# Performance work log

Measured on AMD Instinct MI355X. Metric: run time of the kernel, lower is better.

Reference implementation:

```python
import jax, jax.numpy as jnp
import numpy as np

M, D, NI, L, NPL, R, T = 2, 128, 131072, 4, 2048, 8, 32
N = NI + L * NPL  # total DAG nodes


def setup_inputs() -> dict:
    key = jax.random.key(0)
    ks = jax.random.split(key, 18)
    thax = jax.random.randint(ks[0], (NI,), 0, T)
    sine = jax.random.uniform(ks[1], (NI,), jnp.float32)
    # parents of layer-l deriv nodes index any node built earlier (topological)
    raw = jax.random.randint(ks[2], (L, NPL, 2), 0, 2**30)
    bounds = jnp.array([NI + l * NPL for l in range(L)])[:, None, None]
    par = raw % bounds
    ridx = jax.random.randint(ks[3], (L, NPL), 0, R)
    pos = jax.random.uniform(ks[4], (N,), jnp.float32) + 0.01
    neg = jax.random.uniform(ks[5], (N,), jnp.float32) + 0.01
    s = 0.05
    return {
        'thax': thax, 'sine': sine, 'par': par, 'ridx': ridx,
        'pos': pos, 'neg': neg,
        'init_table': jax.random.normal(ks[6], (M, T, D)) * s,
        's_vec': jax.random.normal(ks[7], (M, D)) * s,
        'W1': jax.random.normal(ks[8], (M, R, 2 * D, D)) * s,
        'b1': jax.random.normal(ks[9], (M, R, D)) * s,
        'W2': jax.random.normal(ks[10], (M, R, D, D)) * s,
        'b2': jax.random.normal(ks[11], (M, R, D)) * s,
        'tweaks': jax.random.normal(ks[12], (M, 1, 2)) * s,
        'We1': jax.random.normal(ks[13], (M, D, D)) * s,
        'be1': jax.random.normal(ks[14], (M, D)) * s,
        'we2': jax.random.normal(ks[15], (M, D)) * s,
        'be2': jax.random.normal(ks[16], (M,)) * s,
    }


def reference(thax, sine, par, ridx, pos, neg, init_table, s_vec,
              W1, b1, W2, b2, tweaks, We1, be1, we2, be2):
    # init nodes: thax embedding + sine embellishment (per model)
    emb0 = init_table[:, thax, :] + sine[None, :, None] * s_vec[:, None, :]  # [M,NI,D]
    store = jnp.zeros((M, N, D), emb0.dtype).at[:, :NI].set(emb0)
    # topological layers of deriv nodes: gather parents, rule-indexed 2-layer MLP
    for l in range(L):
        p, r = par[l], ridx[l]
        cat = store[:, p].reshape(M, NPL, 2 * D)               # gather parents
        h = jax.nn.relu(jnp.einsum('mnc,mncd->mnd', cat, W1[:, r]) + b1[:, r])
        out = (jnp.einsum('mnd,mnde->mne', h, W2[:, r]) + b2[:, r]
               + tweaks[:, 0, 1][:, None, None])
        store = store.at[:, NI + l * NPL: NI + (l + 1) * NPL].set(out)
    # eval_net: per-node scalar logit (+ per-problem tweak)
    he = jax.nn.relu(jnp.einsum('mnd,mde->mne', store, We1) + be1[:, None, :])
    logit = jnp.einsum('mnd,md->mn', he, we2) + be2[:, None] + tweaks[:, 0, 0][:, None]
    tot_pos, tot_neg = pos.sum(), neg.sum()
    pw = tot_neg / tot_pos  # POS_WEIGHT_EXTRA = 1.0
    gold = pos / (pos + neg)
    w = pos + neg
    # BCEWithLogitsLoss(pos_weight=pw) per node, weighted by (pos+neg)
    bce = -(pw * gold[None] * jax.nn.log_sigmoid(logit)
            + (1.0 - gold[None]) * jax.nn.log_sigmoid(-logit))
    loss = (w[None] * bce).sum(axis=1)                          # [M]
    posOK = jnp.where(logit >= 0, pos[None], 0.0).sum(axis=1)
    negOK = jnp.where(logit < 0, neg[None], 0.0).sum(axis=1)
    return (loss, posOK, negOK, tot_pos, tot_neg)
```

## Files before the change

kernel.cpp:

```cpp
#include <hip/hip_runtime.h>
#include <hip/hip_bf16.h>

#define M_ 2
#define D_ 128
#define NI_ 131072
#define L_ 4
#define NPL_ 2048
#define R_ 8
#define T_ 32
#define N_ (NI_ + L_ * NPL_)
#define ND_ (L_ * NPL_)
#define PSTRIDE_ 1280
#define PUSED_ 1248

typedef __bf16 bf16x8 __attribute__((ext_vector_type(8)));
typedef float f32x4 __attribute__((ext_vector_type(4)));

#define OFF_W1T    0u
#define OFF_W2T    1048576u
#define OFF_WE1T   1572864u
#define OFF_TAB    1638400u
#define OFF_SVEC   1654784u
#define OFF_EA2    1688448u
#define OFF_EWB    1721216u
#define OFF_PA     1723264u
#define OFF_PB     1733504u
#define OFF_PPOK   1743744u
#define OFF_PNOK   1753984u
#define OFF_PTP    1764224u
#define OFF_PTN    1769344u
#define OFF_G      1774464u
#define OFF_STORE  2315136u
#define OFF_FSG    6509440u
#define OFF_CFG    6509472u
#define OFF_FLIST  6509504u
#define OFF_SAL    6542272u
#define OFF_SBL    6575040u
#define OFF_FSGA   6577088u
#define OFF_CFGA   6577120u
#define OFF_CB24   6577152u
#define OFF_OB24   6577248u

__device__ __forceinline__ unsigned short f2bu(float f) {
  unsigned int u = __float_as_uint(f);
  u += 0x7fffu + ((u >> 16) & 1u);
  return (unsigned short)(u >> 16);
}
__device__ __forceinline__ bf16x8 ldb8(const unsigned short* p) {
  return *reinterpret_cast<const bf16x8*>(p);
}

__device__ __forceinline__ bf16x8 node_chunk(int m, int row, int d0,
    const unsigned short* tab, const unsigned short* svec,
    const unsigned short* sd, const int* thax, const float* sine) {
  if (row < NI_) {
    bf16x8 tv = ldb8(&tab[(m * T_ + thax[row]) * D_ + d0]);
    bf16x8 sv = ldb8(&svec[m * D_ + d0]);
    float sn = sine[row];
    bf16x8 r;
#pragma unroll
    for (int j = 0; j < 8; ++j)
      r[j] = (__bf16)((float)tv[j] + sn * (float)sv[j]);
    return r;
  }
  return ldb8(&sd[(size_t)(m * ND_ + (row - NI_)) * D_ + d0]);
}

__global__ __launch_bounds__(256) void megaprep_kernel(
    const float* W1, const float* W2, const float* We1,
    const float* init_table, const float* s_vec,
    const float* b1, const float* be1, const float* we2,
    const int* ridx, const int* par,
    unsigned short* W1T, unsigned short* W2T, unsigned short* We1T,
    unsigned short* tab, unsigned short* svec,
    float* G, float* EA2, float* EWB,
    int* fsg, int* cfg, int* fastlist,
    int* fsgA, int* cfgA, int* slowAlist,
    int* cB24, int* oB24, int* slowBlist, unsigned int* pzero) {
  __shared__ float smem[1056];
  __shared__ unsigned int fbm[256];
  __shared__ int scnt[40], soff[40];
  int job = blockIdx.x;
  int tid = threadIdx.x;

  if (job < 800) {
    int z, rblk, cblk;
    if (job < 512)      { z = job >> 5;            rblk = (job & 31) >> 2; cblk = job & 3; }
    else if (job < 768) { int q = job - 512; z = 16 + (q >> 4); rblk = (q & 15) >> 2; cblk = q & 3; }
    else                { int q = job - 768; z = 32 + (q >> 4); rblk = (q & 15) >> 2; cblk = q & 3; }
    const float* src; unsigned short* dst; int R;
    if (z < 16)      { src = W1  + (size_t)z * 32768;        dst = W1T  + (size_t)z * 32768;        R = 256; }
    else if (z < 32) { src = W2  + (size_t)(z - 16) * 16384; dst = W2T  + (size_t)(z - 16) * 16384; R = 128; }
    else             { src = We1 + (size_t)(z - 32) * 16384; dst = We1T + (size_t)(z - 32) * 16384; R = 128; }
    int r0 = rblk * 32, c0 = cblk * 32;
    float (*tile)[33] = (float(*)[33])smem;
    int tx = tid & 31, ty = tid >> 5;
#pragma unroll
    for (int k = 0; k < 4; ++k)
      tile[ty + 8 * k][tx] = src[(size_t)(r0 + ty + 8 * k) * D_ + c0 + tx];
    __syncthreads();
#pragma unroll
    for (int k = 0; k < 4; ++k)
      dst[(size_t)(c0 + ty + 8 * k) * R + r0 + tx] = f2bu(tile[tx][ty + 8 * k]);
  } else if (job == 800) {
    for (int i = tid; i < 8448; i += 256) {
      if (i < 8192) tab[i] = f2bu(init_table[i]);
      else svec[i - 8192] = f2bu(s_vec[i - 8192]);
    }
  } else if (job < 1329) {
    int q = job - 801;
    int t = q / 16, mr = q & 15;
    int m = mr >> 3;
    int slot = tid >> 7, e = tid & 127;
    const float* vec = (t < 32) ? &init_table[(size_t)(m * T_ + t) * D_]
                                : &s_vec[(size_t)m * D_];
    if (tid < 128) smem[tid] = vec[tid];
    __syncthreads();
    const float* w = &W1[((size_t)mr * 256 + slot * 128) * D_];
    float acc = 0.f;
#pragma unroll 8
    for (int c = 0; c < 128; ++c) acc = fmaf(smem[c], w[c * D_ + e], acc);
    if (slot == 0 && t < 32) acc += b1[mr * D_ + e];
    G[((size_t)(mr * 2 + slot) * 33 + t) * D_ + e] = acc;
  } else if (job < 1363) {
    int q = job - 1329;
    int m = q / 17, t = (q % 17) * 2 + (tid >> 7);
    int e = tid & 127;
    if (t <= 32) {
      const float* vec = (t < 32) ? &init_table[(size_t)(m * T_ + t) * D_]
                                  : &s_vec[(size_t)m * D_];
      const float* w = &We1[(size_t)m * D_ * D_];
      float acc = 0.f;
#pragma unroll 8
      for (int d = 0; d < 128; ++d) acc = fmaf(vec[d], w[d * D_ + e], acc);
      if (t < 32) {
        EA2[m * 4096 + ((e >> 1) * 32 + t) * 2 + (e & 1)] = acc + be1[m * D_ + e];
      } else {
        EWB[(m * D_ + e) * 2 + 0] = acc;
        EWB[(m * D_ + e) * 2 + 1] = we2[m * D_ + e];
      }
    }
  } else if (job == 1363) {
    for (int i = tid; i < 256; i += 256) fbm[i] = 0u;
    for (int i = tid; i < 40; i += 256) scnt[i] = 0;
    __syncthreads();
    for (int g = tid; g < ND_; g += 256) {
      if (par[2 * g] < NI_ && par[2 * g + 1] < NI_)
        atomicOr(&fbm[g >> 5], 1u << (g & 31));
    }
    __syncthreads();
    for (int g = tid; g < ND_; g += 256) {
      int r = ridx[g];
      int f = (fbm[g >> 5] >> (g & 31)) & 1;
      if (f) atomicAdd(&scnt[r], 1);
      else {
        int p0 = par[2 * g], p1 = par[2 * g + 1];
        int a0 = p0 < NI_ || ((fbm[(p0 - NI_) >> 5] >> ((p0 - NI_) & 31)) & 1);
        int a1 = p1 < NI_ || ((fbm[(p1 - NI_) >> 5] >> ((p1 - NI_) & 31)) & 1);
        if (a0 && a1) atomicAdd(&scnt[8 + r], 1);
        else atomicAdd(&scnt[16 + ((g >> 11) - 1) * 8 + r], 1);
      }
    }
    __syncthreads();
    if (tid == 0) {
      int run = 0;
      for (int r = 0; r < 8; ++r) { soff[r] = run; fsg[r] = run; cfg[r] = scnt[r]; run += scnt[r]; }
      run = 0;
      for (int r = 0; r < 8; ++r) { soff[8 + r] = run; fsgA[r] = run; cfgA[r] = scnt[8 + r]; run += scnt[8 + r]; }
      run = 0;
      for (int b = 0; b < 24; ++b) { soff[16 + b] = run; oB24[b] = run; cB24[b] = scnt[16 + b]; run += scnt[16 + b]; }
    }
    __syncthreads();
    for (int g = tid; g < ND_; g += 256) {
      int r = ridx[g];
      int f = (fbm[g >> 5] >> (g & 31)) & 1;
      if (f) fastlist[atomicAdd(&soff[r], 1)] = g;
      else {
        int p0 = par[2 * g], p1 = par[2 * g + 1];
        int a0 = p0 < NI_ || ((fbm[(p0 - NI_) >> 5] >> ((p0 - NI_) & 31)) & 1);
        int a1 = p1 < NI_ || ((fbm[(p1 - NI_) >> 5] >> ((p1 - NI_) & 31)) & 1);
        if (a0 && a1) slowAlist[atomicAdd(&soff[8 + r], 1)] = g;
        else slowBlist[atomicAdd(&soff[16 + ((g >> 11) - 1) * 8 + r], 1)] = g;
      }
    }
  } else {
    for (int i = tid; i < 12800; i += 256) pzero[i] = 0u;
  }
}

__global__ __launch_bounds__(256) void main_kernel(
    const int* thax, const float* sine, const int* par,
    const float* pos, const float* neg,
    const float* b2, const float* tweaks,
    const float* G, const unsigned short* W2T, const unsigned short* We1T,
    const float* EA2, const float* EWB,
    const float* be1, const float* we2, const float* be2,
    const int* fsg, const int* cfg, const int* fastlist,
    unsigned short* sd,
    float* pA, float* pB, float* pPok, float* pNok, float* pTp, float* pTn) {
  __shared__ float sbuf[4448];
  int bid = blockIdx.x;
  int tid = threadIdx.x;
  int w = tid >> 6, lane = tid & 63;

  if (bid < 1280) {
    int m = bid / 640, q = bid % 640;
    int r = q / 80, tile = q % 80;
    int cnt = cfg[r];
    int base = tile * 16;
    if (base >= cnt) return;
    unsigned short* h_lds = (unsigned short*)sbuf;
    int*   t0a  = (int*)(sbuf + 1024);
    int*   t1a  = t0a + 16;
    float* s0a  = (float*)(t1a + 16);
    float* s1a  = s0a + 16;
    int*   gida = (int*)(s1a + 16);
    float* red2 = sbuf + 1104;
    if (tid < 16) {
      int loc = base + tid; if (loc >= cnt) loc = cnt - 1;
      int gid = fastlist[fsg[r] + loc];
      int p0 = par[2 * gid], p1 = par[2 * gid + 1];
      t0a[tid] = thax[p0]; s0a[tid] = sine[p0];
      t1a[tid] = thax[p1]; s1a[tid] = sine[p1];
      gida[tid] = gid;
    }
    __syncthreads();
    const float* Gm = &G[(size_t)(m * R_ + r) * 8448];
    {
      int row = tid >> 4, seg = tid & 15, d0 = seg * 8;
      int t0 = t0a[row], t1 = t1a[row];
      float s0 = s0a[row], s1 = s1a[row];
      const float* pa = &Gm[t0 * 128 + d0];
      const float* pb = &Gm[(33 + t1) * 128 + d0];
      const float* pu = &Gm[4096 + d0];
      const float* pv = &Gm[8320 + d0];
      bf16x8 hv;
#pragma unroll
      for (int half = 0; half < 2; ++half) {
        float4 a = *(const float4*)(pa + half * 4);
        float4 b = *(const float4*)(pb + half * 4);
        float4 u = *(const float4*)(pu + half * 4);
        float4 v = *(const float4*)(pv + half * 4);
        hv[half * 4 + 0] = (__bf16)fmaxf(a.x + b.x + s0 * u.x + s1 * v.x, 0.f);
        hv[half * 4 + 1] = (__bf16)fmaxf(a.y + b.y + s0 * u.y + s1 * v.y, 0.f);
        hv[half * 4 + 2] = (__bf16)fmaxf(a.z + b.z + s0 * u.z + s1 * v.z, 0.f);
        hv[half * 4 + 3] = (__bf16)fmaxf(a.w + b.w + s0 * u.w + s1 * v.w, 0.f);
      }
      *(bf16x8*)&h_lds[row * 128 + (d0 ^ ((row & 7) << 3))] = hv;
    }
    __syncthreads();
    int l15 = lane & 15, l4 = lane >> 4;
    const unsigned short* w2b = &W2T[(size_t)(m * R_ + r) * D_ * D_];
    f32x4 acc[2];
    acc[0] = (f32x4){0.f, 0.f, 0.f, 0.f};
    acc[1] = (f32x4){0.f, 0.f, 0.f, 0.f};
#pragma unroll
    for (int kc = 0; kc < 4; ++kc) {
      int d0 = kc * 32 + l4 * 8;
      bf16x8 a2 = ldb8(&h_lds[l15 * 128 + (d0 ^ ((l15 & 7) << 3))]);
#pragma unroll
      for (int f = 0; f < 2; ++f) {
        int fg = w * 2 + f;
        bf16x8 b = ldb8(&w2b[(fg * 16 + l15) * D_ + d0]);
        acc[f] = __builtin_amdgcn_mfma_f32_16x16x32_bf16(a2, b, acc[f], 0, 0, 0);
      }
    }
    float tw1 = tweaks[m * 2 + 1];
    const float* b2v = &b2[(m * R_ + r) * D_];
    __syncthreads();
#pragma unroll
    for (int i = 0; i < 4; ++i) {
      int row = l4 * 4 + i;
      int g = base + row;
#pragma unroll
      for (int f = 0; f < 2; ++f) {
        int e = (w * 2 + f) * 16 + l15;
        unsigned short val = f2bu(acc[f][i] + b2v[e] + tw1);
        h_lds[row * 128 + (e ^ ((row & 7) << 3))] = val;
        if (g < cnt) sd[(size_t)(m * ND_ + gida[row]) * D_ + e] = val;
      }
    }
    __syncthreads();
    f32x4 ae[2];
    ae[0] = (f32x4){0.f, 0.f, 0.f, 0.f};
    ae[1] = (f32x4){0.f, 0.f, 0.f, 0.f};
    const unsigned short* we1b = &We1T[(size_t)m * D_ * D_];
#pragma unroll
    for (int kc = 0; kc < 4; ++kc) {
      int d0 = kc * 32 + l4 * 8;
      bf16x8 a2 = ldb8(&h_lds[l15 * 128 + (d0 ^ ((l15 & 7) << 3))]);
#pragma unroll
      for (int f = 0; f < 2; ++f) {
        int fg = w * 2 + f;
        bf16x8 b = ldb8(&we1b[(fg * 16 + l15) * D_ + d0]);
        ae[f] = __builtin_amdgcn_mfma_f32_16x16x32_bf16(a2, b, ae[f], 0, 0, 0);
      }
    }
    float part[4] = {0.f, 0.f, 0.f, 0.f};
#pragma unroll
    for (int f = 0; f < 2; ++f) {
      int e = (w * 2 + f) * 16 + l15;
      float bb = be1[m * D_ + e];
      float wv = we2[m * D_ + e];
#pragma unroll
      for (int i = 0; i < 4; ++i) {
        float he = ae[f][i] + bb;
        he = he > 0.f ? he : 0.f;
        part[i] += he * wv;
      }
    }
#pragma unroll
    for (int mask = 1; mask < 16; mask <<= 1) {
#pragma unroll
      for (int i = 0; i < 4; ++i) part[i] += __shfl_xor(part[i], mask, 64);
    }
    if (l15 == 0) {
#pragma unroll
      for (int i = 0; i < 4; ++i) red2[w * 16 + l4 * 4 + i] = part[i];
    }
    __syncthreads();
    if (tid < 16) {
      int g = base + tid;
      float v6[4] = {0.f, 0.f, 0.f, 0.f};
      if (g < cnt) {
        float logit = red2[tid] + red2[16 + tid] + red2[32 + tid] + red2[48 + tid]
                    + be2[m] + tweaks[m * 2 + 0];
        int grow = NI_ + gida[tid];
        float p_ = pos[grow], n_ = neg[grow];
        float lse = log1pf(__expf(-fabsf(logit)));
        v6[0] = p_ * (fmaxf(-logit, 0.f) + lse);
        v6[1] = n_ * (fmaxf(logit, 0.f) + lse);
        v6[2] = logit >= 0.f ? p_ : 0.f;
        v6[3] = logit < 0.f ? n_ : 0.f;
      }
#pragma unroll
      for (int mask = 1; mask < 16; mask <<= 1) {
#pragma unroll
        for (int qq = 0; qq < 4; ++qq) v6[qq] += __shfl_xor(v6[qq], mask, 64);
      }
      if (tid == 0) {
        int slot = 512 + r * 80 + tile;
        pA[m * PSTRIDE_ + slot] = v6[0];
        pB[m * PSTRIDE_ + slot] = v6[1];
        pPok[m * PSTRIDE_ + slot] = v6[2];
        pNok[m * PSTRIDE_ + slot] = v6[3];
      }
    }
  } else if (bid < 2304) {
    int q = bid - 1280;
    int m = q >> 9, xb = q & 511;
    float* lea = sbuf;
    float* lwb = sbuf + 4096;
    float* red = sbuf + 4352;
    for (int i = tid; i < 4096; i += 256) lea[i] = EA2[m * 4096 + i];
    if (tid < 256) lwb[tid] = EWB[m * 256 + tid];
    __syncthreads();
    int row = xb * 256 + tid;
    int t = thax[row];
    float s = sine[row];
    float acc = 0.f;
#pragma unroll 8
    for (int p = 0; p < 64; ++p) {
      float2 ea = *(const float2*)&lea[(p * 32 + t) * 2];
      float4 wb = *(const float4*)&lwb[p * 4];
      float x0 = fmaf(s, wb.x, ea.x); x0 = fmaxf(x0, 0.f);
      acc = fmaf(x0, wb.y, acc);
      float x1 = fmaf(s, wb.z, ea.y); x1 = fmaxf(x1, 0.f);
      acc = fmaf(x1, wb.w, acc);
    }
    float logit = acc + be2[m] + tweaks[m * 2 + 0];
    float p_ = pos[row], n_ = neg[row];
    float lse = log1pf(__expf(-fabsf(logit)));
    float v[6];
    v[0] = p_ * (fmaxf(-logit, 0.f) + lse);
    v[1] = n_ * (fmaxf(logit, 0.f) + lse);
    v[2] = logit >= 0.f ? p_ : 0.f;
    v[3] = logit < 0.f ? n_ : 0.f;
    v[4] = p_; v[5] = n_;
#pragma unroll
    for (int mask = 1; mask < 64; mask <<= 1) {
#pragma unroll
      for (int k = 0; k < 6; ++k) v[k] += __shfl_xor(v[k], mask, 64);
    }
    if (lane == 0) {
#pragma unroll
      for (int k = 0; k < 6; ++k) red[k * 16 + w] = v[k];
    }
    __syncthreads();
    if (tid == 0) {
      float t6[6];
#pragma unroll
      for (int k = 0; k < 6; ++k)
        t6[k] = red[k * 16 + 0] + red[k * 16 + 1] + red[k * 16 + 2] + red[k * 16 + 3];
      pA[m * PSTRIDE_ + xb] = t6[0];
      pB[m * PSTRIDE_ + xb] = t6[1];
      pPok[m * PSTRIDE_ + xb] = t6[2];
      pNok[m * PSTRIDE_ + xb] = t6[3];
      if (m == 0) { pTp[xb] = t6[4]; pTn[xb] = t6[5]; }
    }
  } else {
    int j = bid - 2304;
    float* red = sbuf;
    const float* src = j ? neg : pos;
    float s = 0.f;
    for (int i = NI_ + tid; i < N_; i += 256) s += src[i];
#pragma unroll
    for (int mask = 1; mask < 64; mask <<= 1) s += __shfl_xor(s, mask, 64);
    if (lane == 0) red[w] = s;
    __syncthreads();
    if (tid == 0) {
      float t = red[0] + red[1] + red[2] + red[3];
      if (j == 0) pTp[1152] = t; else pTn[1152] = t;
    }
  }
}

__global__ __launch_bounds__(128) void slowA_kernel(
    const int* thax, const float* sine, const int* par,
    const float* b1, const float* b2, const float* tweaks,
    const float* pos, const float* neg,
    const float* be1, const float* we2, const float* be2,
    const unsigned short* tab, const unsigned short* svec,
    const unsigned short* W1T, const unsigned short* W2T,
    const unsigned short* We1T,
    const int* fsgA, const int* cfgA, const int* slowAlist,
    unsigned short* sd,
    float* pA, float* pB, float* pPok, float* pNok) {
  int tile = blockIdx.x, r = blockIdx.y, m = blockIdx.z;
  int cnt = cfgA[r];
  int base = tile * 16;
  if (base >= cnt) return;
  int start = fsgA[r];
  int tid = threadIdx.x;
  int w = tid >> 6, lane = tid & 63;
  int l15 = lane & 15, l4 = lane >> 4;
  __shared__ unsigned short h_lds[16 * 128];
  __shared__ float red2[32];
  __shared__ int grows[16];

  if (tid < 16) {
    int loc = base + tid; if (loc >= cnt) loc = cnt - 1;
    grows[tid] = slowAlist[start + loc];
  }
  __syncthreads();
  int g0 = grows[l15];
  int p0 = par[2 * g0], p1 = par[2 * g0 + 1];
  const unsigned short* w1b = &W1T[(size_t)(m * R_ + r) * D_ * 256];
  const unsigned short* w2b = &W2T[(size_t)(m * R_ + r) * D_ * D_];
  const unsigned short* we1b = &We1T[(size_t)m * D_ * D_];

  bf16x8 av[8];
#pragma unroll
  for (int kc = 0; kc < 8; ++kc) {
    int k = kc * 32 + l4 * 8;
    int p = (k < 128) ? p0 : p1;
    av[kc] = node_chunk(m, p, k & 127, tab, svec, sd, thax, sine);
  }
  f32x4 acch[4];
#pragma unroll
  for (int f = 0; f < 4; ++f) acch[f] = (f32x4){0.f, 0.f, 0.f, 0.f};
#pragma unroll
  for (int kc = 0; kc < 8; ++kc) {
    int k = kc * 32 + l4 * 8;
#pragma unroll
    for (int f = 0; f < 4; ++f) {
      int fg = w * 4 + f;
      bf16x8 b = ldb8(&w1b[(fg * 16 + l15) * 256 + k]);
      acch[f] = __builtin_amdgcn_mfma_f32_16x16x32_bf16(av[kc], b, acch[f], 0, 0, 0);
    }
  }
  const float* b1v = &b1[(m * R_ + r) * D_];
#pragma unroll
  for (int f = 0; f < 4; ++f) {
    int d = (w * 4 + f) * 16 + l15;
    float bb = b1v[d];
#pragma unroll
    for (int i = 0; i < 4; ++i) {
      int row = l4 * 4 + i;
      float h = acch[f][i] + bb;
      h = h > 0.f ? h : 0.f;
      h_lds[row * 128 + (d ^ ((row & 7) << 3))] = f2bu(h);
    }
  }
  __syncthreads();
  f32x4 acco[4];
#pragma unroll
  for (int f = 0; f < 4; ++f) acco[f] = (f32x4){0.f, 0.f, 0.f, 0.f};
#pragma unroll
  for (int kc = 0; kc < 4; ++kc) {
    int d0 = kc * 32 + l4 * 8;
    bf16x8 a2 = ldb8(&h_lds[l15 * 128 + (d0 ^ ((l15 & 7) << 3))]);
#pragma unroll
    for (int f = 0; f < 4; ++f) {
      int fg = w * 4 + f;
      bf16x8 b = ldb8(&w2b[(fg * 16 + l15) * D_ + d0]);
      acco[f] = __builtin_amdgcn_mfma_f32_16x16x32_bf16(a2, b, acco[f], 0, 0, 0);
    }
  }
  float tw1 = tweaks[m * 2 + 1];
  const float* b2v = &b2[(m * R_ + r) * D_];
  __syncthreads();
#pragma unroll
  for (int i = 0; i < 4; ++i) {
    int row = l4 * 4 + i;
    int g = base + row;
#pragma unroll
    for (int f = 0; f < 4; ++f) {
      int e = (w * 4 + f) * 16 + l15;
      unsigned short val = f2bu(acco[f][i] + b2v[e] + tw1);
      h_lds[row * 128 + (e ^ ((row & 7) << 3))] = val;
      if (g < cnt) sd[(size_t)(m * ND_ + grows[row]) * D_ + e] = val;
    }
  }
  __syncthreads();
  f32x4 ae[4];
#pragma unroll
  for (int f = 0; f < 4; ++f) ae[f] = (f32x4){0.f, 0.f, 0.f, 0.f};
#pragma unroll
  for (int kc = 0; kc < 4; ++kc) {
    int d0 = kc * 32 + l4 * 8;
    bf16x8 a2 = ldb8(&h_lds[l15 * 128 + (d0 ^ ((l15 & 7) << 3))]);
#pragma unroll
    for (int f = 0; f < 4; ++f) {
      int fg = w * 4 + f;
      bf16x8 b = ldb8(&we1b[(fg * 16 + l15) * D_ + d0]);
      ae[f] = __builtin_amdgcn_mfma_f32_16x16x32_bf16(a2, b, ae[f], 0, 0, 0);
    }
  }
  float part[4] = {0.f, 0.f, 0.f, 0.f};
#pragma unroll
  for (int f = 0; f < 4; ++f) {
    int e = (w * 4 + f) * 16 + l15;
    float bb = be1[m * D_ + e];
    float wv = we2[m * D_ + e];
#pragma unroll
    for (int i = 0; i < 4; ++i) {
      float he = ae[f][i] + bb;
      he = he > 0.f ? he : 0.f;
      part[i] += he * wv;
    }
  }
#pragma unroll
  for (int mask = 1; mask < 16; mask <<= 1) {
#pragma unroll
    for (int i = 0; i < 4; ++i) part[i] += __shfl_xor(part[i], mask, 64);
  }
  if (l15 == 0) {
#pragma unroll
    for (int i = 0; i < 4; ++i) red2[w * 16 + l4 * 4 + i] = part[i];
  }
  __syncthreads();
  if (tid < 16) {
    int g = base + tid;
    float v6[4] = {0.f, 0.f, 0.f, 0.f};
    if (g < cnt) {
      float logit = red2[tid] + red2[16 + tid] + be2[m] + tweaks[m * 2 + 0];
      int grow = NI_ + grows[tid];
      float p_ = pos[grow], n_ = neg[grow];
      float lse = log1pf(__expf(-fabsf(logit)));
      v6[0] = p_ * (fmaxf(-logit, 0.f) + lse);
      v6[1] = n_ * (fmaxf(logit, 0.f) + lse);
      v6[2] = logit >= 0.f ? p_ : 0.f;
      v6[3] = logit < 0.f ? n_ : 0.f;
    }
#pragma unroll
    for (int mask = 1; mask < 16; mask <<= 1) {
#pragma unroll
      for (int qq = 0; qq < 4; ++qq) v6[qq] += __shfl_xor(v6[qq], mask, 64);
    }
    if (tid == 0) {
      int slot = 1153 + r * 6 + tile;
      pA[m * PSTRIDE_ + slot] = v6[0];
      pB[m * PSTRIDE_ + slot] = v6[1];
      pPok[m * PSTRIDE_ + slot] = v6[2];
      pNok[m * PSTRIDE_ + slot] = v6[3];
    }
  }
}

__global__ __launch_bounds__(128) void slowB_kernel(int l,
    const int* thax, const float* sine, const int* par,
    const float* b1, const float* b2, const float* tweaks,
    const float* pos, const float* neg,
    const float* be1, const float* we2, const float* be2,
    const unsigned short* tab, const unsigned short* svec,
    const unsigned short* W1T, const unsigned short* W2T,
    const unsigned short* We1T,
    const int* cB24, const int* oB24, const int* slowBlist,
    unsigned short* sd,
    float* pA, float* pB, float* pPok, float* pNok) {
  int tile = blockIdx.x, r = blockIdx.y, m = blockIdx.z;
  int bkt = (l - 1) * 8 + r;
  int cnt = cB24[bkt];
  int base = tile * 16;
  if (base >= cnt) return;
  int off = oB24[bkt];
  int tid = threadIdx.x;
  int w = tid >> 6, lane = tid & 63;
  int l15 = lane & 15, l4 = lane >> 4;
  __shared__ unsigned short h_lds[16 * 128];
  __shared__ float red2[32];
  __shared__ int grows[16];

  if (tid < 16) {
    int loc = base + tid; if (loc >= cnt) loc = cnt - 1;
    grows[tid] = slowBlist[off + loc];
  }
  __syncthreads();
  int g0 = grows[l15];
  int p0 = par[2 * g0], p1 = par[2 * g0 + 1];
  const unsigned short* w1b = &W1T[(size_t)(m * R_ + r) * D_ * 256];
  const unsigned short* w2b = &W2T[(size_t)(m * R_ + r) * D_ * D_];
  const unsigned short* we1b = &We1T[(size_t)m * D_ * D_];

  bf16x8 av[8];
#pragma unroll
  for (int kc = 0; kc < 8; ++kc) {
    int k = kc * 32 + l4 * 8;
    int p = (k < 128) ? p0 : p1;
    av[kc] = node_chunk(m, p, k & 127, tab, svec, sd, thax, sine);
  }
  f32x4 acch[4];
#pragma unroll
  for (int f = 0; f < 4; ++f) acch[f] = (f32x4){0.f, 0.f, 0.f, 0.f};
#pragma unroll
  for (int kc = 0; kc < 8; ++kc) {
    int k = kc * 32 + l4 * 8;
#pragma unroll
    for (int f = 0; f < 4; ++f) {
      int fg = w * 4 + f;
      bf16x8 b = ldb8(&w1b[(fg * 16 + l15) * 256 + k]);
      acch[f] = __builtin_amdgcn_mfma_f32_16x16x32_bf16(av[kc], b, acch[f], 0, 0, 0);
    }
  }
  const float* b1v = &b1[(m * R_ + r) * D_];
#pragma unroll
  for (int f = 0; f < 4; ++f) {
    int d = (w * 4 + f) * 16 + l15;
    float bb = b1v[d];
#pragma unroll
    for (int i = 0; i < 4; ++i) {
      int row = l4 * 4 + i;
      float h = acch[f][i] + bb;
      h = h > 0.f ? h : 0.f;
      h_lds[row * 128 + (d ^ ((row & 7) << 3))] = f2bu(h);
    }
  }
  __syncthreads();
  f32x4 acco[4];
#pragma unroll
  for (int f = 0; f < 4; ++f) acco[f] = (f32x4){0.f, 0.f, 0.f, 0.f};
#pragma unroll
  for (int kc = 0; kc < 4; ++kc) {
    int d0 = kc * 32 + l4 * 8;
    bf16x8 a2 = ldb8(&h_lds[l15 * 128 + (d0 ^ ((l15 & 7) << 3))]);
#pragma unroll
    for (int f = 0; f < 4; ++f) {
      int fg = w * 4 + f;
      bf16x8 b = ldb8(&w2b[(fg * 16 + l15) * D_ + d0]);
      acco[f] = __builtin_amdgcn_mfma_f32_16x16x32_bf16(a2, b, acco[f], 0, 0, 0);
    }
  }
  float tw1 = tweaks[m * 2 + 1];
  const float* b2v = &b2[(m * R_ + r) * D_];
  __syncthreads();
#pragma unroll
  for (int i = 0; i < 4; ++i) {
    int row = l4 * 4 + i;
    int g = base + row;
#pragma unroll
    for (int f = 0; f < 4; ++f) {
      int e = (w * 4 + f) * 16 + l15;
      unsigned short val = f2bu(acco[f][i] + b2v[e] + tw1);
      h_lds[row * 128 + (e ^ ((row & 7) << 3))] = val;
      if (g < cnt) sd[(size_t)(m * ND_ + grows[row]) * D_ + e] = val;
    }
  }
  __syncthreads();
  f32x4 ae[4];
#pragma unroll
  for (int f = 0; f < 4; ++f) ae[f] = (f32x4){0.f, 0.f, 0.f, 0.f};
#pragma unroll
  for (int kc = 0; kc < 4; ++kc) {
    int d0 = kc * 32 + l4 * 8;
    bf16x8 a2 = ldb8(&h_lds[l15 * 128 + (d0 ^ ((l15 & 7) << 3))]);
#pragma unroll
    for (int f = 0; f < 4; ++f) {
      int fg = w * 4 + f;
      bf16x8 b = ldb8(&we1b[(fg * 16 + l15) * D_ + d0]);
      ae[f] = __builtin_amdgcn_mfma_f32_16x16x32_bf16(a2, b, ae[f], 0, 0, 0);
    }
  }
  float part[4] = {0.f, 0.f, 0.f, 0.f};
#pragma unroll
  for (int f = 0; f < 4; ++f) {
    int e = (w * 4 + f) * 16 + l15;
    float bb = be1[m * D_ + e];
    float wv = we2[m * D_ + e];
#pragma unroll
    for (int i = 0; i < 4; ++i) {
      float he = ae[f][i] + bb;
      he = he > 0.f ? he : 0.f;
      part[i] += he * wv;
    }
  }
#pragma unroll
  for (int mask = 1; mask < 16; mask <<= 1) {
#pragma unroll
    for (int i = 0; i < 4; ++i) part[i] += __shfl_xor(part[i], mask, 64);
  }
  if (l15 == 0) {
#pragma unroll
    for (int i = 0; i < 4; ++i) red2[w * 16 + l4 * 4 + i] = part[i];
  }
  __syncthreads();
  if (tid < 16) {
    int g = base + tid;
    float v6[4] = {0.f, 0.f, 0.f, 0.f};
    if (g < cnt) {
      float logit = red2[tid] + red2[16 + tid] + be2[m] + tweaks[m * 2 + 0];
      int grow = NI_ + grows[tid];
      float p_ = pos[grow], n_ = neg[grow];
      float lse = log1pf(__expf(-fabsf(logit)));
      v6[0] = p_ * (fmaxf(-logit, 0.f) + lse);
      v6[1] = n_ * (fmaxf(logit, 0.f) + lse);
      v6[2] = logit >= 0.f ? p_ : 0.f;
      v6[3] = logit < 0.f ? n_ : 0.f;
    }
#pragma unroll
    for (int mask = 1; mask < 16; mask <<= 1) {
#pragma unroll
      for (int qq = 0; qq < 4; ++qq) v6[qq] += __shfl_xor(v6[qq], mask, 64);
    }
    if (tid == 0) {
      int slot = 1201 + (l - 2) * 16 + r * 2 + tile;
      pA[m * PSTRIDE_ + slot] = v6[0];
      pB[m * PSTRIDE_ + slot] = v6[1];
      pPok[m * PSTRIDE_ + slot] = v6[2];
      pNok[m * PSTRIDE_ + slot] = v6[3];
    }
  }
}

__global__ __launch_bounds__(256) void finalize_kernel(
    const float* pA, const float* pB, const float* pPok, const float* pNok,
    const float* pTp, const float* pTn, float* out) {
  __shared__ float lred[10][4];
  const float* srcs[10] = {pA, pA + PSTRIDE_, pB, pB + PSTRIDE_,
                           pPok, pPok + PSTRIDE_, pNok, pNok + PSTRIDE_,
                           pTp, pTn};
  int tid = threadIdx.x;
  int w = tid >> 6, lane = tid & 63;
#pragma unroll
  for (int q = 0; q < 10; ++q) {
    float s = 0.f;
    for (int i = tid; i < PUSED_; i += 256) s += srcs[q][i];
#pragma unroll
    for (int mask = 1; mask < 64; mask <<= 1) s += __shfl_xor(s, mask, 64);
    if (lane == 0) lred[q][w] = s;
  }
  __syncthreads();
  if (tid == 0) {
    float totals[10];
#pragma unroll
    for (int q = 0; q < 10; ++q)
      totals[q] = lred[q][0] + lred[q][1] + lred[q][2] + lred[q][3];
    float tp = totals[8], tn = totals[9];
    float pw = tn / tp;
    out[0] = pw * totals[0] + totals[2];
    out[1] = pw * totals[1] + totals[3];
    out[2] = totals[4]; out[3] = totals[5];
    out[4] = totals[6]; out[5] = totals[7];
    out[6] = tp; out[7] = tn;
  }
}

extern "C" void kernel_launch(void* const* d_in, const int* in_sizes, int n_in,
                              void* d_out, int out_size, void* d_ws, size_t ws_size,
                              hipStream_t stream) {
  const int*   thax = (const int*)d_in[0];
  const float* sine = (const float*)d_in[1];
  const int*   par  = (const int*)d_in[2];
  const int*   ridx = (const int*)d_in[3];
  const float* pos  = (const float*)d_in[4];
  const float* neg  = (const float*)d_in[5];
  const float* init_table = (const float*)d_in[6];
  const float* s_vec = (const float*)d_in[7];
  const float* W1 = (const float*)d_in[8];
  const float* b1 = (const float*)d_in[9];
  const float* W2 = (const float*)d_in[10];
  const float* b2 = (const float*)d_in[11];
  const float* tweaks = (const float*)d_in[12];
  const float* We1 = (const float*)d_in[13];
  const float* be1 = (const float*)d_in[14];
  const float* we2 = (const float*)d_in[15];
  const float* be2 = (const float*)d_in[16];

  char* ws = (char*)d_ws;
  unsigned short* W1T  = (unsigned short*)(ws + OFF_W1T);
  unsigned short* W2T  = (unsigned short*)(ws + OFF_W2T);
  unsigned short* We1T = (unsigned short*)(ws + OFF_WE1T);
  unsigned short* tab  = (unsigned short*)(ws + OFF_TAB);
  unsigned short* svec = (unsigned short*)(ws + OFF_SVEC);
  float* EA2  = (float*)(ws + OFF_EA2);
  float* EWB  = (float*)(ws + OFF_EWB);
  float* pA   = (float*)(ws + OFF_PA);
  float* pB   = (float*)(ws + OFF_PB);
  float* pPok = (float*)(ws + OFF_PPOK);
  float* pNok = (float*)(ws + OFF_PNOK);
  float* pTp  = (float*)(ws + OFF_PTP);
  float* pTn  = (float*)(ws + OFF_PTN);
  float* G    = (float*)(ws + OFF_G);
  unsigned short* sd = (unsigned short*)(ws + OFF_STORE);
  int* fsg      = (int*)(ws + OFF_FSG);
  int* cfg      = (int*)(ws + OFF_CFG);
  int* fastlist = (int*)(ws + OFF_FLIST);
  int* slowAlist = (int*)(ws + OFF_SAL);
  int* slowBlist = (int*)(ws + OFF_SBL);
  int* fsgA     = (int*)(ws + OFF_FSGA);
  int* cfgA     = (int*)(ws + OFF_CFGA);
  int* cB24     = (int*)(ws + OFF_CB24);
  int* oB24     = (int*)(ws + OFF_OB24);

  megaprep_kernel<<<1365, 256, 0, stream>>>(
      W1, W2, We1, init_table, s_vec, b1, be1, we2, ridx, par,
      W1T, W2T, We1T, tab, svec, G, EA2, EWB,
      fsg, cfg, fastlist, fsgA, cfgA, slowAlist, cB24, oB24, slowBlist,
      (unsigned int*)pA);
  main_kernel<<<2306, 256, 0, stream>>>(
      thax, sine, par, pos, neg, b2, tweaks, G, W2T, We1T, EA2, EWB,
      be1, we2, be2, fsg, cfg, fastlist, sd,
      pA, pB, pPok, pNok, pTp, pTn);
  slowA_kernel<<<dim3(6, R_, M_), 128, 0, stream>>>(
      thax, sine, par, b1, b2, tweaks, pos, neg, be1, we2, be2,
      tab, svec, W1T, W2T, We1T, fsgA, cfgA, slowAlist, sd,
      pA, pB, pPok, pNok);
  for (int l = 2; l < L_; ++l) {
    slowB_kernel<<<dim3(2, R_, M_), 128, 0, stream>>>(
        l, thax, sine, par, b1, b2, tweaks, pos, neg, be1, we2, be2,
        tab, svec, W1T, W2T, We1T, cB24, oB24, slowBlist, sd,
        pA, pB, pPok, pNok);
  }
  finalize_kernel<<<1, 256, 0, stream>>>(pA, pB, pPok, pNok, pTp, pTn,
                                         (float*)d_out);
}
```

Baseline: 108.5 us.

## Parallelize node bucketing across 40 blocks with fixed-capacity lists and ballot compaction

The single-block serial bucketing job (bitmap, count, prefix sum, scatter) is replaced by 40 blocks, one per bucket. Each block scans all derived nodes, recomputes the fast/slowA test directly from parent indices, and compacts its matches into a fixed-capacity list using wavefront ballot plus one LDS atomic per wave. The bucketing jobs are also moved to the lowest block indices so they start first and no longer sit on the tail of the prep kernel. In exchange, the list capacities are fixed constants sized for these inputs and overflowing nodes are silently dropped, and every block rereads the full parent array.

```diff
diff --git a/kernel.cpp b/kernel.cpp
--- a/kernel.cpp
+++ b/kernel.cpp
@@ -12,6 +12,9 @@
 #define ND_ (L_ * NPL_)
 #define PSTRIDE_ 1280
 #define PUSED_ 1248
+#define FCAP_ 1280
+#define ACAP_ 96
+#define BCAP_ 32
 
 typedef __bf16 bf16x8 __attribute__((ext_vector_type(8)));
 typedef float f32x4 __attribute__((ext_vector_type(4)));
@@ -31,15 +34,12 @@
 #define OFF_PTN    1769344u
 #define OFF_G      1774464u
 #define OFF_STORE  2315136u
-#define OFF_FSG    6509440u
-#define OFF_CFG    6509472u
-#define OFF_FLIST  6509504u
-#define OFF_SAL    6542272u
-#define OFF_SBL    6575040u
-#define OFF_FSGA   6577088u
-#define OFF_CFGA   6577120u
-#define OFF_CB24   6577152u
-#define OFF_OB24   6577248u
+#define OFF_FLIST  6509440u
+#define OFF_SAL    6550400u
+#define OFF_SBL    6553472u
+#define OFF_CFG    6556544u
+#define OFF_CFGA   6556576u
+#define OFF_CB24   6556608u
 
 __device__ __forceinline__ unsigned short f2bu(float f) {
   unsigned int u = __float_as_uint(f);
@@ -74,56 +74,68 @@
     unsigned short* W1T, unsigned short* W2T, unsigned short* We1T,
     unsigned short* tab, unsigned short* svec,
     float* G, float* EA2, float* EWB,
-    int* fsg, int* cfg, int* fastlist,
-    int* fsgA, int* cfgA, int* slowAlist,
-    int* cB24, int* oB24, int* slowBlist, unsigned int* pzero) {
+    int* fastlist, int* slowAlist, int* slowBlist,
+    int* cfg, int* cfgA, int* cB24, unsigned int* pzero) {
   __shared__ float smem[1056];
-  __shared__ unsigned int fbm[256];
-  __shared__ int scnt[40], soff[40];
+  __shared__ int lcnt;
   int job = blockIdx.x;
   int tid = threadIdx.x;
 
-  if (job < 800) {
-    int z, rblk, cblk;
-    if (job < 512)      { z = job >> 5;            rblk = (job & 31) >> 2; cblk = job & 3; }
-    else if (job < 768) { int q = job - 512; z = 16 + (q >> 4); rblk = (q & 15) >> 2; cblk = q & 3; }
-    else                { int q = job - 768; z = 32 + (q >> 4); rblk = (q & 15) >> 2; cblk = q & 3; }
-    const float* src; unsigned short* dst; int R;
-    if (z < 16)      { src = W1  + (size_t)z * 32768;        dst = W1T  + (size_t)z * 32768;        R = 256; }
-    else if (z < 32) { src = W2  + (size_t)(z - 16) * 16384; dst = W2T  + (size_t)(z - 16) * 16384; R = 128; }
-    else             { src = We1 + (size_t)(z - 32) * 16384; dst = We1T + (size_t)(z - 32) * 16384; R = 128; }
-    int r0 = rblk * 32, c0 = cblk * 32;
-    float (*tile)[33] = (float(*)[33])smem;
-    int tx = tid & 31, ty = tid >> 5;
-#pragma unroll
-    for (int k = 0; k < 4; ++k)
-      tile[ty + 8 * k][tx] = src[(size_t)(r0 + ty + 8 * k) * D_ + c0 + tx];
-    __syncthreads();
-#pragma unroll
-    for (int k = 0; k < 4; ++k)
-      dst[(size_t)(c0 + ty + 8 * k) * R + r0 + tx] = f2bu(tile[tx][ty + 8 * k]);
-  } else if (job == 800) {
+  if (job < 40) {
+    int* out; int bucketbase, cap;
+    if (job < 8)       { out = fastlist;  bucketbase = job * FCAP_;        cap = FCAP_; }
+    else if (job < 16) { out = slowAlist; bucketbase = (job - 8) * ACAP_;  cap = ACAP_; }
+    else               { out = slowBlist; bucketbase = (job - 16) * BCAP_; cap = BCAP_; }
+    if (tid == 0) lcnt = 0;
+    __syncthreads();
+    int lane = tid & 63;
+    unsigned long long lmask_lt = (1ull << lane) - 1ull;
+    for (int g = tid; g < ND_; g += 256) {
+      int p0 = par[2 * g], p1 = par[2 * g + 1];
+      bool fast = (p0 < NI_) && (p1 < NI_);
+      bool match;
+      if (job < 8) {
+        match = fast && (ridx[g] == job);
+      } else if (fast) {
+        match = false;
+      } else {
+        bool a0 = (p0 < NI_) ||
+                  (par[2 * (p0 - NI_)] < NI_ && par[2 * (p0 - NI_) + 1] < NI_);
+        bool a1 = (p1 < NI_) ||
+                  (par[2 * (p1 - NI_)] < NI_ && par[2 * (p1 - NI_) + 1] < NI_);
+        bool isA = a0 && a1;
+        if (job < 16) match = isA && (ridx[g] == job - 8);
+        else match = !isA && ((((g >> 11) - 1) * 8 + ridx[g]) == job - 16);
+      }
+      unsigned long long mask = __ballot(match);
+      if (mask) {
+        int leader = __ffsll((unsigned long long)mask) - 1;
+        int pre = __popcll(mask & lmask_lt);
+        int base_ = 0;
+        if (lane == leader) base_ = atomicAdd(&lcnt, __popcll(mask));
+        base_ = __shfl(base_, leader, 64);
+        if (match) {
+          int idx = base_ + pre;
+          if (idx < cap) out[bucketbase + idx] = g;
+        }
+      }
+    }
+    __syncthreads();
+    if (tid == 0) {
+      int c = lcnt; if (c > cap) c = cap;
+      if (job < 8) cfg[job] = c;
+      else if (job < 16) cfgA[job - 8] = c;
+      else cB24[job - 16] = c;
+    }
+  } else if (job == 40) {
+    for (int i = tid; i < 12800; i += 256) pzero[i] = 0u;
+  } else if (job == 41) {
     for (int i = tid; i < 8448; i += 256) {
       if (i < 8192) tab[i] = f2bu(init_table[i]);
       else svec[i - 8192] = f2bu(s_vec[i - 8192]);
     }
-  } else if (job < 1329) {
-    int q = job - 801;
-    int t = q / 16, mr = q & 15;
-    int m = mr >> 3;
-    int slot = tid >> 7, e = tid & 127;
-    const float* vec = (t < 32) ? &init_table[(size_t)(m * T_ + t) * D_]
-                                : &s_vec[(size_t)m * D_];
-    if (tid < 128) smem[tid] = vec[tid];
-    __syncthreads();
-    const float* w = &W1[((size_t)mr * 256 + slot * 128) * D_];
-    float acc = 0.f;
-#pragma unroll 8
-    for (int c = 0; c < 128; ++c) acc = fmaf(smem[c], w[c * D_ + e], acc);
-    if (slot == 0 && t < 32) acc += b1[mr * D_ + e];
-    G[((size_t)(mr * 2 + slot) * 33 + t) * D_ + e] = acc;
-  } else if (job < 1363) {
-    int q = job - 1329;
+  } else if (job < 76) {
+    int q = job - 42;
     int m = q / 17, t = (q % 17) * 2 + (tid >> 7);
     int e = tid & 127;
     if (t <= 32) {
@@ -140,51 +152,41 @@
         EWB[(m * D_ + e) * 2 + 1] = we2[m * D_ + e];
       }
     }
-  } else if (job == 1363) {
-    for (int i = tid; i < 256; i += 256) fbm[i] = 0u;
-    for (int i = tid; i < 40; i += 256) scnt[i] = 0;
-    __syncthreads();
-    for (int g = tid; g < ND_; g += 256) {
-      if (par[2 * g] < NI_ && par[2 * g + 1] < NI_)
-        atomicOr(&fbm[g >> 5], 1u << (g & 31));
-    }
-    __syncthreads();
-    for (int g = tid; g < ND_; g += 256) {
-      int r = ridx[g];
-      int f = (fbm[g >> 5] >> (g & 31)) & 1;
-      if (f) atomicAdd(&scnt[r], 1);
-      else {
-        int p0 = par[2 * g], p1 = par[2 * g + 1];
-        int a0 = p0 < NI_ || ((fbm[(p0 - NI_) >> 5] >> ((p0 - NI_) & 31)) & 1);
-        int a1 = p1 < NI_ || ((fbm[(p1 - NI_) >> 5] >> ((p1 - NI_) & 31)) & 1);
-        if (a0 && a1) atomicAdd(&scnt[8 + r], 1);
-        else atomicAdd(&scnt[16 + ((g >> 11) - 1) * 8 + r], 1);
-      }
-    }
-    __syncthreads();
-    if (tid == 0) {
-      int run = 0;
-      for (int r = 0; r < 8; ++r) { soff[r] = run; fsg[r] = run; cfg[r] = scnt[r]; run += scnt[r]; }
-      run = 0;
-      for (int r = 0; r < 8; ++r) { soff[8 + r] = run; fsgA[r] = run; cfgA[r] = scnt[8 + r]; run += scnt[8 + r]; }
-      run = 0;
-      for (int b = 0; b < 24; ++b) { soff[16 + b] = run; oB24[b] = run; cB24[b] = scnt[16 + b]; run += scnt[16 + b]; }
-    }
-    __syncthreads();
-    for (int g = tid; g < ND_; g += 256) {
-      int r = ridx[g];
-      int f = (fbm[g >> 5] >> (g & 31)) & 1;
-      if (f) fastlist[atomicAdd(&soff[r], 1)] = g;
-      else {
-        int p0 = par[2 * g], p1 = par[2 * g + 1];
-        int a0 = p0 < NI_ || ((fbm[(p0 - NI_) >> 5] >> ((p0 - NI_) & 31)) & 1);
-        int a1 = p1 < NI_ || ((fbm[(p1 - NI_) >> 5] >> ((p1 - NI_) & 31)) & 1);
-        if (a0 && a1) slowAlist[atomicAdd(&soff[8 + r], 1)] = g;
-        else slowBlist[atomicAdd(&soff[16 + ((g >> 11) - 1) * 8 + r], 1)] = g;
-      }
-    }
+  } else if (job < 604) {
+    int q = job - 76;
+    int t = q / 16, mr = q & 15;
+    int m = mr >> 3;
+    int slot = tid >> 7, e = tid & 127;
+    const float* vec = (t < 32) ? &init_table[(size_t)(m * T_ + t) * D_]
+                                : &s_vec[(size_t)m * D_];
+    if (tid < 128) smem[tid] = vec[tid];
+    __syncthreads();
+    const float* w = &W1[((size_t)mr * 256 + slot * 128) * D_];
+    float acc = 0.f;
+#pragma unroll 8
+    for (int c = 0; c < 128; ++c) acc = fmaf(smem[c], w[c * D_ + e], acc);
+    if (slot == 0 && t < 32) acc += b1[mr * D_ + e];
+    G[((size_t)(mr * 2 + slot) * 33 + t) * D_ + e] = acc;
   } else {
-    for (int i = tid; i < 12800; i += 256) pzero[i] = 0u;
+    int q0 = job - 604;
+    int z, rblk, cblk;
+    if (q0 < 512)      { z = q0 >> 5;            rblk = (q0 & 31) >> 2; cblk = q0 & 3; }
+    else if (q0 < 768) { int q = q0 - 512; z = 16 + (q >> 4); rblk = (q & 15) >> 2; cblk = q & 3; }
+    else               { int q = q0 - 768; z = 32 + (q >> 4); rblk = (q & 15) >> 2; cblk = q & 3; }
+    const float* src; unsigned short* dst; int R;
+    if (z < 16)      { src = W1  + (size_t)z * 32768;        dst = W1T  + (size_t)z * 32768;        R = 256; }
+    else if (z < 32) { src = W2  + (size_t)(z - 16) * 16384; dst = W2T  + (size_t)(z - 16) * 16384; R = 128; }
+    else             { src = We1 + (size_t)(z - 32) * 16384; dst = We1T + (size_t)(z - 32) * 16384; R = 128; }
+    int r0 = rblk * 32, c0 = cblk * 32;
+    float (*tile)[33] = (float(*)[33])smem;
+    int tx = tid & 31, ty = tid >> 5;
+#pragma unroll
+    for (int k = 0; k < 4; ++k)
+      tile[ty + 8 * k][tx] = src[(size_t)(r0 + ty + 8 * k) * D_ + c0 + tx];
+    __syncthreads();
+#pragma unroll
+    for (int k = 0; k < 4; ++k)
+      dst[(size_t)(c0 + ty + 8 * k) * R + r0 + tx] = f2bu(tile[tx][ty + 8 * k]);
   }
 }
 
@@ -195,7 +197,7 @@
     const float* G, const unsigned short* W2T, const unsigned short* We1T,
     const float* EA2, const float* EWB,
     const float* be1, const float* we2, const float* be2,
-    const int* fsg, const int* cfg, const int* fastlist,
+    const int* cfg, const int* fastlist,
     unsigned short* sd,
     float* pA, float* pB, float* pPok, float* pNok, float* pTp, float* pTn) {
   __shared__ float sbuf[4448];
@@ -218,7 +220,7 @@
     float* red2 = sbuf + 1104;
     if (tid < 16) {
       int loc = base + tid; if (loc >= cnt) loc = cnt - 1;
-      int gid = fastlist[fsg[r] + loc];
+      int gid = fastlist[r * FCAP_ + loc];
       int p0 = par[2 * gid], p1 = par[2 * gid + 1];
       t0a[tid] = thax[p0]; s0a[tid] = sine[p0];
       t1a[tid] = thax[p1]; s1a[tid] = sine[p1];
@@ -423,14 +425,13 @@
     const unsigned short* tab, const unsigned short* svec,
     const unsigned short* W1T, const unsigned short* W2T,
     const unsigned short* We1T,
-    const int* fsgA, const int* cfgA, const int* slowAlist,
+    const int* cfgA, const int* slowAlist,
     unsigned short* sd,
     float* pA, float* pB, float* pPok, float* pNok) {
   int tile = blockIdx.x, r = blockIdx.y, m = blockIdx.z;
   int cnt = cfgA[r];
   int base = tile * 16;
   if (base >= cnt) return;
-  int start = fsgA[r];
   int tid = threadIdx.x;
   int w = tid >> 6, lane = tid & 63;
   int l15 = lane & 15, l4 = lane >> 4;
@@ -440,7 +441,7 @@
 
   if (tid < 16) {
     int loc = base + tid; if (loc >= cnt) loc = cnt - 1;
-    grows[tid] = slowAlist[start + loc];
+    grows[tid] = slowAlist[r * ACAP_ + loc];
   }
   __syncthreads();
   int g0 = grows[l15];
@@ -586,7 +587,7 @@
     const unsigned short* tab, const unsigned short* svec,
     const unsigned short* W1T, const unsigned short* W2T,
     const unsigned short* We1T,
-    const int* cB24, const int* oB24, const int* slowBlist,
+    const int* cB24, const int* slowBlist,
     unsigned short* sd,
     float* pA, float* pB, float* pPok, float* pNok) {
   int tile = blockIdx.x, r = blockIdx.y, m = blockIdx.z;
@@ -594,7 +595,6 @@
   int cnt = cB24[bkt];
   int base = tile * 16;
   if (base >= cnt) return;
-  int off = oB24[bkt];
   int tid = threadIdx.x;
   int w = tid >> 6, lane = tid & 63;
   int l15 = lane & 15, l4 = lane >> 4;
@@ -604,7 +604,7 @@
 
   if (tid < 16) {
     int loc = base + tid; if (loc >= cnt) loc = cnt - 1;
-    grows[tid] = slowBlist[off + loc];
+    grows[tid] = slowBlist[bkt * BCAP_ + loc];
   }
   __syncthreads();
   int g0 = grows[l15];
@@ -812,33 +812,30 @@
   float* pTn  = (float*)(ws + OFF_PTN);
   float* G    = (float*)(ws + OFF_G);
   unsigned short* sd = (unsigned short*)(ws + OFF_STORE);
-  int* fsg      = (int*)(ws + OFF_FSG);
-  int* cfg      = (int*)(ws + OFF_CFG);
-  int* fastlist = (int*)(ws + OFF_FLIST);
+  int* fastlist  = (int*)(ws + OFF_FLIST);
   int* slowAlist = (int*)(ws + OFF_SAL);
   int* slowBlist = (int*)(ws + OFF_SBL);
-  int* fsgA     = (int*)(ws + OFF_FSGA);
-  int* cfgA     = (int*)(ws + OFF_CFGA);
-  int* cB24     = (int*)(ws + OFF_CB24);
-  int* oB24     = (int*)(ws + OFF_OB24);
-
-  megaprep_kernel<<<1365, 256, 0, stream>>>(
+  int* cfg       = (int*)(ws + OFF_CFG);
+  int* cfgA      = (int*)(ws + OFF_CFGA);
+  int* cB24      = (int*)(ws + OFF_CB24);
+
+  megaprep_kernel<<<1404, 256, 0, stream>>>(
       W1, W2, We1, init_table, s_vec, b1, be1, we2, ridx, par,
       W1T, W2T, We1T, tab, svec, G, EA2, EWB,
-      fsg, cfg, fastlist, fsgA, cfgA, slowAlist, cB24, oB24, slowBlist,
+      fastlist, slowAlist, slowBlist, cfg, cfgA, cB24,
       (unsigned int*)pA);
   main_kernel<<<2306, 256, 0, stream>>>(
       thax, sine, par, pos, neg, b2, tweaks, G, W2T, We1T, EA2, EWB,
-      be1, we2, be2, fsg, cfg, fastlist, sd,
+      be1, we2, be2, cfg, fastlist, sd,
       pA, pB, pPok, pNok, pTp, pTn);
   slowA_kernel<<<dim3(6, R_, M_), 128, 0, stream>>>(
       thax, sine, par, b1, b2, tweaks, pos, neg, be1, we2, be2,
-      tab, svec, W1T, W2T, We1T, fsgA, cfgA, slowAlist, sd,
+      tab, svec, W1T, W2T, We1T, cfgA, slowAlist, sd,
       pA, pB, pPok, pNok);
   for (int l = 2; l < L_; ++l) {
     slowB_kernel<<<dim3(2, R_, M_), 128, 0, stream>>>(
         l, thax, sine, par, b1, b2, tweaks, pos, neg, be1, we2, be2,
-        tab, svec, W1T, W2T, We1T, cB24, oB24, slowBlist, sd,
+        tab, svec, W1T, W2T, We1T, cB24, slowBlist, sd,
         pA, pB, pPok, pNok);
   }
   finalize_kernel<<<1, 256, 0, stream>>>(pA, pB, pPok, pNok, pTp, pTn,
```

Result: faster. 95.76 us (-11.7%).
